# Performance work log

Measured on AMD Instinct MI355X. Metric: run time of the kernel, lower is better.

## Reference

```python
import jax, jax.numpy as jnp
import numpy as np

NEG = -1.0e30  # log-space 'zero' that is safe in fp32
EPS = 1e-7     # keras.backend.ctc_batch_cost epsilon


def setup_inputs() -> dict:
    key = jax.random.key(0)
    k1, k2 = jax.random.split(key)
    B, T, C, L = 256, 512, 256, 128
    # y_pred are post-softmax probabilities, as expected by ctc_batch_cost
    logits = jax.random.normal(k1, (B, T, C), dtype=jnp.float32)
    y_pred = jax.nn.softmax(logits, axis=-1)
    # labels in [0, C-1): never equal to blank index C-1
    y_true = jax.random.randint(k2, (B, L), 0, C - 1, dtype=jnp.int32)
    return {"y_true": y_true, "y_pred": y_pred}


def _ctc_batch_cost(y_true, y_pred):
    """Faithful keras.backend.ctc_batch_cost with full input/label lengths.

    y_true: [B, L] int labels (no blanks). y_pred: [B, T, C] probabilities.
    Blank index = C - 1 (TF v1 ctc_loss convention). Returns [B, 1] loss.
    """
    B, T, C = y_pred.shape
    L = y_true.shape[1]
    blank = C - 1
    S = 2 * L + 1  # extended label: blank, l0, blank, l1, ..., blank

    logp = jnp.log(y_pred + EPS)                                # [B, T, C]
    ext = jnp.full((B, S), blank, dtype=y_true.dtype).at[:, 1::2].set(y_true)
    # per-(t, s) log prob of the extended symbol
    lp = jnp.take_along_axis(logp, ext[:, None, :].astype(jnp.int32), axis=2)  # [B, T, S]

    # skip transition s-2 -> s allowed iff s >= 2, ext[s] != blank, ext[s] != ext[s-2]
    ext_m2 = jnp.pad(ext, ((0, 0), (2, 0)), constant_values=blank)[:, :S]
    skip = (ext != blank) & (ext != ext_m2) & (jnp.arange(S)[None, :] >= 2)

    # alpha init at t=0: only s=0 (blank) and s=1 (first label) reachable
    alpha0 = jnp.where(jnp.arange(S)[None, :] < 2, lp[:, 0, :], NEG)  # [B, S]

    def step(alpha, lp_t):
        p1 = jnp.pad(alpha, ((0, 0), (1, 0)), constant_values=NEG)[:, :S]
        p2 = jnp.pad(alpha, ((0, 0), (2, 0)), constant_values=NEG)[:, :S]
        a = jnp.logaddexp(alpha, p1)
        a = jnp.logaddexp(a, jnp.where(skip, p2, NEG))
        return a + lp_t, None

    lp_time_major = jnp.moveaxis(lp, 1, 0)  # [T, B, S]
    alpha, _ = jax.lax.scan(step, alpha0, lp_time_major[1:])
    # total log-likelihood ends at last blank or last label
    loss = -jnp.logaddexp(alpha[:, S - 1], alpha[:, S - 2])    # [B]
    return loss[:, None]                                        # [B, 1]


def reference(y_true, y_pred):
    # CTCLayer.call computes ctc_batch_cost with input_length = T, label_length = L
    # for every batch row, adds it as a loss, and passes y_pred through. The
    # compute of interest is the loss itself, returned here as [B, 1].
    return _ctc_batch_cost(y_true, y_pred)
```

## Files before the change

### kernel.cpp

```cpp
#include <hip/hip_runtime.h>
#include <math.h>


namespace {
constexpr int Bn = 256;
constexpr int Tn = 512;
constexpr int Cn = 256;
constexpr int Ln = 128;
constexpr int U  = 8;
constexpr int NC = Tn / U;
constexpr float EPSf = 1e-7f;
constexpr float LN2f = 0.69314718055994530942f;
constexpr int   TGT  = 60;
}

__global__ __launch_bounds__(64, 1)
void ctc_fwd(const int* __restrict__ y_true,
             const float* __restrict__ y_pred,
             float* __restrict__ out)
{
    const int b    = blockIdx.x;
    const int lane = threadIdx.x;

    const int* yt = y_true + b * Ln;
    const int l0 = yt[2 * lane];
    const int l1 = yt[2 * lane + 1];
    const int lm = (lane > 0) ? yt[2 * lane - 1] : -1;
    const float sk1 = (lane > 0 && l0 != lm) ? 1.0f : 0.0f;
    const float sk3 = (l1 != l0) ? 1.0f : 0.0f;

    const float* __restrict__ base = y_pred + (size_t)b * Tn * Cn;

    float a0 = (lane == 0) ? 1.0f : 0.0f;
    float a1 = 0.0f, a2 = 0.0f, a3 = 0.0f, a4 = 0.0f;
    int Eacc = 0;

    float vb[4][U], v0[4][U], v1[4][U];

    auto load_chunk = [&](int c, float* bb, float* b0, float* b1) {
        const float* rp = base + (size_t)c * U * Cn;
        #pragma unroll
        for (int u = 0; u < U; ++u) {
            bb[u] = rp[u * Cn + (Cn - 1)];
            b0[u] = rp[u * Cn + l0];
            b1[u] = rp[u * Cn + l1];
        }
    };

    auto compute_chunk = [&](const float* bb, const float* b0, const float* b1) {
        #pragma unroll
        for (int u = 0; u < U; ++u) {
            float n = __shfl_up(a3, 1);
            if (lane == 0) n = 0.0f;
            const float Pb = bb[u] + EPSf;
            const float P0 = b0[u] + EPSf;
            const float P1 = b1[u] + EPSf;
            const float na0 = (a0 + n) * Pb;
            const float na1 = fmaf(sk1, n,  a1 + a0) * P0;
            const float na2 = (a2 + a1) * Pb;
            const float na3 = fmaf(sk3, a1, a3 + a2) * P1;
            const float na4 = (a4 + a3) * Pb;
            a0 = na0; a1 = na1; a2 = na2; a3 = na3; a4 = na4;
        }
        float m = fmaxf(fmaxf(fmaxf(a0, a1), fmaxf(a2, a3)), a4);
        #pragma unroll
        for (int off = 32; off >= 1; off >>= 1)
            m = fmaxf(m, __shfl_xor(m, off));
        int e;
        (void)frexpf(m, &e);
        const int shift = TGT - e;
        a0 = ldexpf(a0, shift);
        a1 = ldexpf(a1, shift);
        a2 = ldexpf(a2, shift);
        a3 = ldexpf(a3, shift);
        a4 = ldexpf(a4, shift);
        Eacc -= shift;
    };

    load_chunk(0, vb[0], v0[0], v1[0]);
    load_chunk(1, vb[1], v0[1], v1[1]);
    load_chunk(2, vb[2], v0[2], v1[2]);

    for (int c = 0; c < NC; c += 4) {
        if (c + 3 < NC) load_chunk(c + 3, vb[3], v0[3], v1[3]);
        compute_chunk(vb[0], v0[0], v1[0]);
        if (c + 4 < NC) load_chunk(c + 4, vb[0], v0[0], v1[0]);
        compute_chunk(vb[1], v0[1], v1[1]);
        if (c + 5 < NC) load_chunk(c + 5, vb[1], v0[1], v1[1]);
        compute_chunk(vb[2], v0[2], v1[2]);
        if (c + 6 < NC) load_chunk(c + 6, vb[2], v0[2], v1[2]);
        compute_chunk(vb[3], v0[3], v1[3]);
    }

    if (lane == 63) {
        const float s = a3 + a4;
        out[b] = -LN2f * (log2f(s) + (float)Eacc);
    }
}

extern "C" void kernel_launch(void* const* d_in, const int* in_sizes, int n_in,
                              void* d_out, int out_size, void* d_ws, size_t ws_size,
                              hipStream_t stream) {
    const int*   y_true = (const int*)  d_in[0];
    const float* y_pred = (const float*)d_in[1];
    float* out = (float*)d_out;
    (void)in_sizes; (void)n_in; (void)out_size; (void)d_ws; (void)ws_size;
    ctc_fwd<<<dim3(Bn), dim3(64), 0, stream>>>(y_true, y_pred, out);
}
```

Baseline: 243.3 us.

## Stream full rows with coalesced dwordx4 loads and gather labels via bpermute

Each timestep's row of 256 probabilities is now loaded whole, with one coalesced 16-byte load per lane, replacing the three scattered per-lane scalar gathers. The needed label and blank values are picked out with ds_bpermute and readlane. A deep 32-slot register ring of in-flight loads is driven by inline asm and manual vmcnt waits to hide memory latency on this serial recurrence. This reads the full row rather than three values, so it moves more bytes. It also adds eight cross-lane permutes per step to the critical path, and relies on waitcnt semantics that the compiler cannot see.

```diff
diff --git a/kernel.cpp b/kernel.cpp
--- a/kernel.cpp
+++ b/kernel.cpp
@@ -7,11 +7,23 @@
 constexpr int Tn = 512;
 constexpr int Cn = 256;
 constexpr int Ln = 128;
-constexpr int U  = 8;
-constexpr int NC = Tn / U;
+constexpr int D  = 32;
 constexpr float EPSf = 1e-7f;
 constexpr float LN2f = 0.69314718055994530942f;
 constexpr int   TGT  = 60;
+}
+
+typedef float f4 __attribute__((ext_vector_type(4)));
+
+#define GLOAD(dst, p) \
+    asm volatile("global_load_dwordx4 %0, %1, off" : "=v"(dst) : "v"(p))
+#define WAITP(dst) \
+    asm volatile("s_waitcnt vmcnt(31)" : "+v"(dst))
+#define WAIT0(dst) \
+    asm volatile("s_waitcnt vmcnt(0)" : "+v"(dst))
+
+__device__ __forceinline__ float bpf(int idx4, float v) {
+    return __int_as_float(__builtin_amdgcn_ds_bpermute(idx4, __float_as_int(v)));
 }
 
 __global__ __launch_bounds__(64, 1)
@@ -28,40 +40,40 @@
     const int lm = (lane > 0) ? yt[2 * lane - 1] : -1;
     const float sk1 = (lane > 0 && l0 != lm) ? 1.0f : 0.0f;
     const float sk3 = (l1 != l0) ? 1.0f : 0.0f;
+    const float lzm = (lane > 0) ? 1.0f : 0.0f;
 
-    const float* __restrict__ base = y_pred + (size_t)b * Tn * Cn;
+    const int i0 = (l0 >> 2) << 2;
+    const int i1 = (l1 >> 2) << 2;
+    const bool s0a = l0 & 1, s0b = l0 & 2;
+    const bool s1a = l1 & 1, s1b = l1 & 2;
 
     float a0 = (lane == 0) ? 1.0f : 0.0f;
     float a1 = 0.0f, a2 = 0.0f, a3 = 0.0f, a4 = 0.0f;
     int Eacc = 0;
 
-    float vb[4][U], v0[4][U], v1[4][U];
+    auto step = [&](f4 r) {
+        float x0 = bpf(i0, r.x), x1 = bpf(i0, r.y);
+        float x2 = bpf(i0, r.z), x3 = bpf(i0, r.w);
+        float y0 = bpf(i1, r.x), y1 = bpf(i1, r.y);
+        float y2 = bpf(i1, r.z), y3 = bpf(i1, r.w);
+        float v0 = s0b ? (s0a ? x3 : x2) : (s0a ? x1 : x0);
+        float v1 = s1b ? (s1a ? y3 : y2) : (s1a ? y1 : y0);
+        float bb = __int_as_float(
+            __builtin_amdgcn_readlane(__float_as_int(r.w), 63));
 
-    auto load_chunk = [&](int c, float* bb, float* b0, float* b1) {
-        const float* rp = base + (size_t)c * U * Cn;
-        #pragma unroll
-        for (int u = 0; u < U; ++u) {
-            bb[u] = rp[u * Cn + (Cn - 1)];
-            b0[u] = rp[u * Cn + l0];
-            b1[u] = rp[u * Cn + l1];
-        }
+        float n  = __shfl_up(a3, 1) * lzm;
+        const float Pb = bb + EPSf;
+        const float P0 = v0 + EPSf;
+        const float P1 = v1 + EPSf;
+        const float na0 = (a0 + n) * Pb;
+        const float na1 = fmaf(sk1, n,  a1 + a0) * P0;
+        const float na2 = (a2 + a1) * Pb;
+        const float na3 = fmaf(sk3, a1, a3 + a2) * P1;
+        const float na4 = (a4 + a3) * Pb;
+        a0 = na0; a1 = na1; a2 = na2; a3 = na3; a4 = na4;
     };
 
-    auto compute_chunk = [&](const float* bb, const float* b0, const float* b1) {
-        #pragma unroll
-        for (int u = 0; u < U; ++u) {
-            float n = __shfl_up(a3, 1);
-            if (lane == 0) n = 0.0f;
-            const float Pb = bb[u] + EPSf;
-            const float P0 = b0[u] + EPSf;
-            const float P1 = b1[u] + EPSf;
-            const float na0 = (a0 + n) * Pb;
-            const float na1 = fmaf(sk1, n,  a1 + a0) * P0;
-            const float na2 = (a2 + a1) * Pb;
-            const float na3 = fmaf(sk3, a1, a3 + a2) * P1;
-            const float na4 = (a4 + a3) * Pb;
-            a0 = na0; a1 = na1; a2 = na2; a3 = na3; a4 = na4;
-        }
+    auto rescale = [&]() {
         float m = fmaxf(fmaxf(fmaxf(a0, a1), fmaxf(a2, a3)), a4);
         #pragma unroll
         for (int off = 32; off >= 1; off >>= 1)
@@ -77,19 +89,26 @@
         Eacc -= shift;
     };
 
-    load_chunk(0, vb[0], v0[0], v1[0]);
-    load_chunk(1, vb[1], v0[1], v1[1]);
-    load_chunk(2, vb[2], v0[2], v1[2]);
+    const float* p = y_pred + (size_t)b * Tn * Cn + lane * 4;
+    f4 buf[D];
 
-    for (int c = 0; c < NC; c += 4) {
-        if (c + 3 < NC) load_chunk(c + 3, vb[3], v0[3], v1[3]);
-        compute_chunk(vb[0], v0[0], v1[0]);
-        if (c + 4 < NC) load_chunk(c + 4, vb[0], v0[0], v1[0]);
-        compute_chunk(vb[1], v0[1], v1[1]);
-        if (c + 5 < NC) load_chunk(c + 5, vb[1], v0[1], v1[1]);
-        compute_chunk(vb[2], v0[2], v1[2]);
-        if (c + 6 < NC) load_chunk(c + 6, vb[2], v0[2], v1[2]);
-        compute_chunk(vb[3], v0[3], v1[3]);
+    #pragma unroll
+    for (int j = 0; j < D; ++j) { GLOAD(buf[j], p); p += Cn; }
+
+    for (int c = 0; c < Tn - D; c += D) {
+        #pragma unroll
+        for (int j = 0; j < D; ++j) {
+            WAITP(buf[j]);
+            step(buf[j]);
+            GLOAD(buf[j], p); p += Cn;
+            if ((j & 7) == 7) rescale();
+        }
+    }
+    #pragma unroll
+    for (int j = 0; j < D; ++j) {
+        WAIT0(buf[j]);
+        step(buf[j]);
+        if ((j & 7) == 7) rescale();
     }
 
     if (lane == 63) {
```

Result: faster. 210.3 us (-13.6%).
